# Kernel tuning notes

Hardware: AMD Instinct MI355X
Metric: run time of the kernel (lower is better)

The kernel has to match this reference:

```python
import jax, jax.numpy as jnp
import numpy as np

N_NODES = 20000
N_EDGES = 160000
IN_SIZE = 128
HIDDEN = 256
N_HID_LAYERS = 2
OUT_SIZE = 32
N_GRAPHS = 16
NUM_MP = 4  # BASELINE_MESSAGE_PASSING (weights SHARED across rounds: [Sequential(...)]*N)
NEG_SLOPE = 0.01  # torch.nn.LeakyReLU default
W_SCALE = 0.05


def leaky(x):
    return jnp.where(x >= 0, x, NEG_SLOPE * x)


def wide_mlp(h, Win, bin_, Wh, bh, Wout, bout):
    # Linear(in,H) + act, then N_HID_LAYERS x (Linear(H,H) + act), then Linear(H,out)
    h = leaky(h @ Win + bin_)
    for l in range(Wh.shape[0]):  # small fixed layer count
        h = leaky(h @ Wh[l] + bh[l])
    return h @ Wout + bout


def setup_inputs() -> dict:
    key = jax.random.key(0)
    ks = jax.random.split(key, 16)
    d = {
        "x": jax.random.normal(ks[0], (N_NODES, IN_SIZE), jnp.float32),
        "edge_index": jax.random.randint(ks[1], (2, N_EDGES), 0, N_NODES, jnp.int64),
        "batch": jnp.sort(jax.random.randint(ks[2], (N_NODES,), 0, N_GRAPHS, jnp.int64)),
        "enc_Win": W_SCALE * jax.random.normal(ks[3], (IN_SIZE, HIDDEN), jnp.float32),
        "enc_bin": jnp.zeros((HIDDEN,), jnp.float32),
        "enc_Wh": W_SCALE * jax.random.normal(ks[4], (N_HID_LAYERS, HIDDEN, HIDDEN), jnp.float32),
        "enc_bh": jnp.zeros((N_HID_LAYERS, HIDDEN), jnp.float32),
        "enc_Wout": W_SCALE * jax.random.normal(ks[5], (HIDDEN, HIDDEN), jnp.float32),
        "enc_bout": jnp.zeros((HIDDEN,), jnp.float32),
        "edge_W": W_SCALE * jax.random.normal(ks[6], (3 * HIDDEN, HIDDEN), jnp.float32),
        "edge_b": jnp.zeros((HIDDEN,), jnp.float32),
        "proc_Win": W_SCALE * jax.random.normal(ks[7], (HIDDEN, HIDDEN), jnp.float32),
        "proc_bin": jnp.zeros((HIDDEN,), jnp.float32),
        "proc_Wh": W_SCALE * jax.random.normal(ks[8], (N_HID_LAYERS, HIDDEN, HIDDEN), jnp.float32),
        "proc_bh": jnp.zeros((N_HID_LAYERS, HIDDEN), jnp.float32),
        "proc_Wout": W_SCALE * jax.random.normal(ks[9], (HIDDEN, HIDDEN), jnp.float32),
        "proc_bout": jnp.zeros((HIDDEN,), jnp.float32),
        "dec_Win": W_SCALE * jax.random.normal(ks[10], (3 * HIDDEN, HIDDEN), jnp.float32),
        "dec_bin": jnp.zeros((HIDDEN,), jnp.float32),
        "dec_Wh": W_SCALE * jax.random.normal(ks[11], (N_HID_LAYERS, HIDDEN, HIDDEN), jnp.float32),
        "dec_bh": jnp.zeros((N_HID_LAYERS, HIDDEN), jnp.float32),
        "dec_Wout": W_SCALE * jax.random.normal(ks[12], (HIDDEN, OUT_SIZE), jnp.float32),
        "dec_bout": jnp.zeros((OUT_SIZE,), jnp.float32),
    }
    return d


def reference(x, edge_index, batch,
              enc_Win, enc_bin, enc_Wh, enc_bh, enc_Wout, enc_bout,
              edge_W, edge_b,
              proc_Win, proc_bin, proc_Wh, proc_bh, proc_Wout, proc_bout,
              dec_Win, dec_bin, dec_Wh, dec_bh, dec_Wout, dec_bout):
    n = x.shape[0]
    # encode
    h = wide_mlp(x, enc_Win, enc_bin, enc_Wh, enc_bh, enc_Wout, enc_bout)
    # add_self_loops
    loops = jnp.arange(n, dtype=edge_index.dtype)
    ei = jnp.concatenate([edge_index, jnp.stack([loops, loops])], axis=1)
    src, dst = ei[0], ei[1]  # PyG: j = ei[0] (source), i = ei[1] (target/aggregation index)
    e = jnp.zeros((ei.shape[1], HIDDEN), h.dtype)  # edge_attr None branch -> zeros
    # BASELINE_MESSAGE_PASSING rounds, shared weights
    for _ in range(NUM_MP):
        m = jnp.concatenate([h[dst], h[src], e], axis=-1) @ edge_W + edge_b  # [E+N, H]
        h = jax.ops.segment_sum(m, dst, num_segments=n)  # aggr='add'
        h = wide_mlp(h, proc_Win, proc_bin, proc_Wh, proc_bh, proc_Wout, proc_bout)
    # global mean / max / add pooling over graphs
    sums = jax.ops.segment_sum(h, batch, num_segments=N_GRAPHS)
    cnt = jax.ops.segment_sum(jnp.ones((n, 1), h.dtype), batch, num_segments=N_GRAPHS)
    mean = sums / jnp.maximum(cnt, 1.0)
    mx = jax.ops.segment_max(h, batch, num_segments=N_GRAPHS)
    pooled = jnp.concatenate([mean, mx, sums], axis=-1)  # [G, 3H]
    out = wide_mlp(pooled, dec_Win, dec_bin, dec_Wh, dec_bh, dec_Wout, dec_bout)
    return out
```

## Files before the change

### kernel.cpp

```cpp
#include <hip/hip_runtime.h>
#include <hip/hip_bf16.h>
#include <cstdint>

#define HID 256
#define NGRAPH 16
#define NEG_SLOPE 0.01f

typedef __bf16 bf16x8 __attribute__((ext_vector_type(8)));
typedef float f32x4 __attribute__((ext_vector_type(4)));

__device__ __forceinline__ float leaky(float x) { return x >= 0.f ? x : NEG_SLOPE * x; }

__device__ __forceinline__ ushort f2b(float f) {
  uint u = __float_as_uint(f);
  uint r = (u + 0x7fffu + ((u >> 16) & 1u)) >> 16;
  return (ushort)r;
}
__device__ __forceinline__ float b2f(ushort b) { return __uint_as_float((uint)b << 16); }

__global__ __launch_bounds__(256) void k_zero_i32(int* p, int n) {
  int i = blockIdx.x * blockDim.x + threadIdx.x;
  if (i < n) p[i] = 0;
}

__global__ __launch_bounds__(256) void k_hist(const int* __restrict__ key, int* __restrict__ cnt, int ne) {
  int e = blockIdx.x * blockDim.x + threadIdx.x;
  if (e < ne) atomicAdd(&cnt[key[e]], 1);
}

__global__ __launch_bounds__(1024) void k_scan(const int* __restrict__ cnt, int* __restrict__ rowptr,
                                               int* __restrict__ cursor, int n) {
  __shared__ int sd[1024];
  int tid = threadIdx.x;
  int CH = n / 1024 + 1;
  int base = tid * CH;
  int s = 0;
  for (int i = 0; i < CH; ++i) { int idx = base + i; if (idx < n) s += cnt[idx]; }
  sd[tid] = s;
  __syncthreads();
  for (int off = 1; off < 1024; off <<= 1) {
    int v = (tid >= off) ? sd[tid - off] : 0;
    __syncthreads();
    sd[tid] += v;
    __syncthreads();
  }
  int run = (tid == 0) ? 0 : sd[tid - 1];
  for (int i = 0; i < CH; ++i) {
    int idx = base + i;
    if (idx <= n) {
      rowptr[idx] = run;
      if (idx < n) { cursor[idx] = run; run += cnt[idx]; }
    }
  }
}

__global__ __launch_bounds__(64) void k_gbounds(const int* __restrict__ batch, int n,
                                                int* __restrict__ gstart, int* __restrict__ gcnt) {
  int t = threadIdx.x;
  if (t <= NGRAPH) {
    int lo = 0, hi = n;
    while (lo < hi) { int mid = (lo + hi) >> 1; if (batch[mid] < t) lo = mid + 1; else hi = mid; }
    gstart[t] = lo;
  }
  __syncthreads();
  if (t < NGRAPH) gcnt[t] = gstart[t + 1] - gstart[t];
}

__global__ __launch_bounds__(256) void k_scatter(const int* __restrict__ src, const int* __restrict__ dst,
                                                 int* __restrict__ cursor, int* __restrict__ col, int ne) {
  int e = blockIdx.x * blockDim.x + threadIdx.x;
  if (e < ne) {
    int d = dst[e];
    int pos = atomicAdd(&cursor[d], 1);
    col[pos] = src[e];
  }
}

__global__ __launch_bounds__(256) void k_f2b(const float* __restrict__ src, ushort* __restrict__ dst, int nElem) {
  int i = (blockIdx.x * 256 + threadIdx.x) * 4;
  if (i + 3 < nElem) {
    float4 v = *(const float4*)&src[i];
    ushort4 o;
    o.x = f2b(v.x); o.y = f2b(v.y); o.z = f2b(v.z); o.w = f2b(v.w);
    *(ushort4*)&dst[i] = o;
  } else {
    for (int j = i; j < nElem; ++j) dst[j] = f2b(src[j]);
  }
}

struct WconvArgs {
  const float* src[9];
  ushort* dst[9];
  int K[9];
};

__global__ __launch_bounds__(256) void k_wconv_all(WconvArgs args) {
  __shared__ float t[32][33];
  const int e = blockIdx.z;
  const int K = args.K[e];
  const int k0 = blockIdx.x * 32;
  if (k0 >= K) return;
  const float* src = args.src[e];
  ushort* dst = args.dst[e];
  const int n0 = blockIdx.y * 32;
  const int tx = threadIdx.x & 31;
  const int ty = threadIdx.x >> 5;
#pragma unroll
  for (int r = 0; r < 4; ++r) t[ty + 8 * r][tx] = src[(size_t)(k0 + ty + 8 * r) * 256 + n0 + tx];
  __syncthreads();
#pragma unroll
  for (int r = 0; r < 4; ++r) dst[(size_t)(n0 + ty + 8 * r) * K + k0 + tx] = f2b(t[tx][ty + 8 * r]);
}

__global__ __launch_bounds__(256) void k_aggregate(const ushort* __restrict__ h, const int* __restrict__ rowptr,
                                                   const int* __restrict__ col, ushort* __restrict__ S,
                                                   ushort* __restrict__ hd, float* __restrict__ degf, int n) {
  int node = blockIdx.x * 4 + (threadIdx.x >> 6);
  if (node >= n) return;
  int lane = threadIdx.x & 63;
  const ushort4* h4 = (const ushort4*)h;
  size_t base = (size_t)node * 64 + lane;
  ushort4 self = h4[base];
  float a0 = b2f(self.x), a1 = b2f(self.y), a2 = b2f(self.z), a3 = b2f(self.w);
  float s0 = a0, s1 = a1, s2 = a2, s3 = a3;
  int beg = rowptr[node], end = rowptr[node + 1];
  int p = beg;
  for (; p + 4 <= end; p += 4) {
    int j0 = col[p], j1 = col[p + 1], j2 = col[p + 2], j3 = col[p + 3];
    ushort4 v0 = h4[(size_t)j0 * 64 + lane];
    ushort4 v1 = h4[(size_t)j1 * 64 + lane];
    ushort4 v2 = h4[(size_t)j2 * 64 + lane];
    ushort4 v3 = h4[(size_t)j3 * 64 + lane];
    s0 += b2f(v0.x) + b2f(v1.x) + b2f(v2.x) + b2f(v3.x);
    s1 += b2f(v0.y) + b2f(v1.y) + b2f(v2.y) + b2f(v3.y);
    s2 += b2f(v0.z) + b2f(v1.z) + b2f(v2.z) + b2f(v3.z);
    s3 += b2f(v0.w) + b2f(v1.w) + b2f(v2.w) + b2f(v3.w);
  }
  for (; p < end; ++p) {
    int j = col[p];
    ushort4 v = h4[(size_t)j * 64 + lane];
    s0 += b2f(v.x); s1 += b2f(v.y); s2 += b2f(v.z); s3 += b2f(v.w);
  }
  float deg = (float)(end - beg + 1);
  ushort4 so; so.x = f2b(s0); so.y = f2b(s1); so.z = f2b(s2); so.w = f2b(s3);
  ((ushort4*)S)[base] = so;
  ushort4 ho; ho.x = f2b(deg * a0); ho.y = f2b(deg * a1); ho.z = f2b(deg * a2); ho.w = f2b(deg * a3);
  ((ushort4*)hd)[base] = ho;
  if (lane == 0) degf[node] = deg;
}

struct MLPArgs {
  const ushort* A0;
  const ushort* A1;
  const ushort* W0b;
  const ushort* W[5];
  const float* bias[5];
  const float* degf;
  ushort* out;
  int ldw0;
  int actf[5];
};

template <int NL, int K0, bool DUAL>
__global__ __launch_bounds__(256, 2) void k_mlp(MLPArgs args, int M) {
  __shared__ ushort act[8 * 64 * 32];
  __shared__ __align__(16) ushort As[2][64 * 32];
  __shared__ __align__(16) ushort Bs[2][256 * 32];
  __shared__ float degs[64];

  const int m0 = blockIdx.x * 64;
  const int tid = threadIdx.x;
  const int lane = tid & 63;
  const int wn = tid >> 6;
  const int rl = lane & 15;
  const int kg = lane >> 4;

  if (DUAL && tid < 64) {
    int rr = m0 + tid; if (rr > M - 1) rr = M - 1;
    degs[tid] = args.degf[rr];
  }

  const int s_row = tid >> 2;
  const int s_kg = (tid & 3) ^ ((s_row >> 1) & 3);
  int ga = m0 + s_row; if (ga > M - 1) ga = M - 1;

#define STAGE_A(buf, Ap, k0s)                                                            \
  {                                                                                      \
    const ushort* sa_ = (Ap) + (size_t)ga * K0 + (k0s) + s_kg * 8;                       \
    __builtin_amdgcn_global_load_lds(                                                    \
        (const __attribute__((address_space(1))) void*)sa_,                              \
        (__attribute__((address_space(3))) void*)&As[buf][tid * 8], 16, 0, 0);           \
  }
#define STAGE_B(buf, Wp, ldw, k0s)                                                       \
  _Pragma("unroll")                                                                      \
  for (int i_ = 0; i_ < 4; ++i_) {                                                       \
    const ushort* sb_ = (Wp) + (size_t)(s_row + 64 * i_) * (ldw) + (k0s) + s_kg * 8;     \
    __builtin_amdgcn_global_load_lds(                                                    \
        (const __attribute__((address_space(1))) void*)sb_,                              \
        (__attribute__((address_space(3))) void*)&Bs[buf][(tid + 256 * i_) * 8], 16, 0, 0); \
  }

  int rr_[4], sA_[4], rn_[4], sB_[4];
#pragma unroll
  for (int fm = 0; fm < 4; ++fm) {
    rr_[fm] = fm * 16 + rl;
    sA_[fm] = kg ^ ((rr_[fm] >> 1) & 3);
  }
#pragma unroll
  for (int fn = 0; fn < 4; ++fn) {
    rn_[fn] = wn * 64 + fn * 16 + rl;
    sB_[fn] = kg ^ ((rn_[fn] >> 1) & 3);
  }

  f32x4 acc[4][4];

  auto epilogue = [&](int L, bool toGlobal) {
    const float* bp = args.bias[L];
    const int af_ = args.actf[L];
#pragma unroll
    for (int fn = 0; fn < 4; ++fn) {
      int c = wn * 64 + fn * 16 + rl;
      float bv = bp[c];
      int ch = c >> 5, g = (c >> 3) & 3, e = c & 7;
#pragma unroll
      for (int fm = 0; fm < 4; ++fm) {
        int lrow0 = fm * 16 + kg * 4;
#pragma unroll
        for (int rg = 0; rg < 4; ++rg) {
          int lrow = lrow0 + rg;
          float rs = (DUAL && L == 0) ? degs[lrow] : 1.0f;
          float v = acc[fm][fn][rg] + rs * bv;
          if (af_) v = leaky(v);
          if (toGlobal) {
            int grow = m0 + lrow;
            if (grow < M) args.out[(size_t)grow * 256 + c] = f2b(v);
          } else {
            int slot = g ^ ((lrow >> 1) & 3);
            act[ch * 2048 + lrow * 32 + slot * 8 + e] = f2b(v);
          }
        }
      }
    }
  };

  constexpr int KS0 = K0 >> 5;
  constexpr int NT0 = DUAL ? 2 * KS0 : KS0;
#pragma unroll
  for (int i = 0; i < 4; ++i)
#pragma unroll
    for (int j = 0; j < 4; ++j) acc[i][j] = (f32x4)(0.f);

  STAGE_A(0, args.A0, 0);
  STAGE_B(0, args.W[0], args.ldw0, 0);
  __syncthreads();

#pragma unroll
  for (int t = 0; t < NT0; ++t) {
    if (t + 1 < NT0) {
      const int tp = t + 1;
      const int pass = DUAL ? (tp >= KS0 ? 1 : 0) : 0;
      const int k0s = (tp - pass * KS0) << 5;
      const ushort* Ap = pass ? args.A1 : args.A0;
      const ushort* Wp = pass ? args.W0b : args.W[0];
      STAGE_A(tp & 1, Ap, k0s);
      STAGE_B(tp & 1, Wp, args.ldw0, k0s);
    } else if (NL > 1) {
      STAGE_B(0, args.W[1], 256, 0);
    }
    const ushort* bA = &As[t & 1][0];
    const ushort* bB = &Bs[t & 1][0];
    bf16x8 afr[4], bfr[4];
#pragma unroll
    for (int fm = 0; fm < 4; ++fm) afr[fm] = *(const bf16x8*)&bA[rr_[fm] * 32 + sA_[fm] * 8];
#pragma unroll
    for (int fn = 0; fn < 4; ++fn) bfr[fn] = *(const bf16x8*)&bB[rn_[fn] * 32 + sB_[fn] * 8];
#pragma unroll
    for (int fm = 0; fm < 4; ++fm)
#pragma unroll
      for (int fn = 0; fn < 4; ++fn)
        acc[fm][fn] = __builtin_amdgcn_mfma_f32_16x16x32_bf16(afr[fm], bfr[fn], acc[fm][fn], 0, 0, 0);
    __syncthreads();
  }
  epilogue(0, NL == 1);
  if (NL > 1) __syncthreads();

  for (int L = 1; L < NL; ++L) {
#pragma unroll
    for (int i = 0; i < 4; ++i)
#pragma unroll
      for (int j = 0; j < 4; ++j) acc[i][j] = (f32x4)(0.f);
#pragma unroll
    for (int t = 0; t < 8; ++t) {
      if (t < 7) {
        STAGE_B((t + 1) & 1, args.W[L], 256, (t + 1) * 32);
      } else if (L + 1 < NL) {
        STAGE_B(0, args.W[L + 1], 256, 0);
      }
      const ushort* bB = &Bs[t & 1][0];
      bf16x8 afr[4], bfr[4];
#pragma unroll
      for (int fm = 0; fm < 4; ++fm)
        afr[fm] = *(const bf16x8*)&act[t * 2048 + rr_[fm] * 32 + sA_[fm] * 8];
#pragma unroll
      for (int fn = 0; fn < 4; ++fn) bfr[fn] = *(const bf16x8*)&bB[rn_[fn] * 32 + sB_[fn] * 8];
#pragma unroll
      for (int fm = 0; fm < 4; ++fm)
#pragma unroll
        for (int fn = 0; fn < 4; ++fn)
          acc[fm][fn] = __builtin_amdgcn_mfma_f32_16x16x32_bf16(afr[fm], bfr[fn], acc[fm][fn], 0, 0, 0);
      __syncthreads();
    }
    if (L == NL - 1) {
      epilogue(L, true);
    } else {
      epilogue(L, false);
      __syncthreads();
    }
  }
#undef STAGE_A
#undef STAGE_B
}

__global__ __launch_bounds__(256) void k_dec_layer(
    const float* __restrict__ A, const float* __restrict__ W,
    const float* __restrict__ bias, float* __restrict__ out,
    int K, int N, int act)
{
  __shared__ float a[768];
  __shared__ float red[8][64];
  const int g = blockIdx.y;
  const int cols = (N >= 64) ? 64 : 32;
  const int segs = 256 / cols;
  const int t = threadIdx.x;
  const int col = t % cols, seg = t / cols;
  const int c = blockIdx.x * cols + col;
  for (int i = t; i < K; i += 256) a[i] = A[(size_t)g * K + i];
  __syncthreads();
  const int kper = K / segs;
  const int k0 = seg * kper;
  float p = 0.f;
#pragma unroll 8
  for (int k = k0; k < k0 + kper; ++k) p += a[k] * W[(size_t)k * N + c];
  red[seg][col] = p;
  __syncthreads();
  if (seg == 0) {
    float s = bias[c];
    for (int i = 0; i < segs; ++i) s += red[i][col];
    out[(size_t)g * N + c] = act ? leaky(s) : s;
  }
}

__global__ __launch_bounds__(256) void k_pool1(const ushort* __restrict__ h, const int* __restrict__ gstart,
                                               const int* __restrict__ gcnt, float* __restrict__ psum,
                                               float* __restrict__ pmax) {
  int g = blockIdx.x >> 4;
  int cch = blockIdx.x & 15;
  int t = threadIdx.x;
  int len = gcnt[g];
  int s0 = gstart[g];
  int chunk = (len + 15) >> 4;
  int i0 = s0 + cch * chunk;
  int i1 = min(i0 + chunk, s0 + len);
  float s = 0.f;
  float m = -3.402823466e+38f;
  for (int i = i0; i < i1; ++i) {
    float v = b2f(h[(size_t)i * HID + t]);
    s += v;
    m = fmaxf(m, v);
  }
  psum[(size_t)blockIdx.x * HID + t] = s;
  pmax[(size_t)blockIdx.x * HID + t] = m;
}

__global__ __launch_bounds__(256) void k_pool2(const float* __restrict__ psum, const float* __restrict__ pmax,
                                               const int* __restrict__ gcnt, float* __restrict__ pooled) {
  int g = blockIdx.x;
  int t = threadIdx.x;
  float s = 0.f, m = -3.402823466e+38f;
  for (int cch = 0; cch < 16; ++cch) {
    s += psum[(size_t)(g * 16 + cch) * HID + t];
    m = fmaxf(m, pmax[(size_t)(g * 16 + cch) * HID + t]);
  }
  float cf = (float)gcnt[g];
  pooled[g * 3 * HID + t] = s / fmaxf(cf, 1.f);
  pooled[g * 3 * HID + HID + t] = m;
  pooled[g * 3 * HID + 2 * HID + t] = s;
}

extern "C" void kernel_launch(void* const* d_in, const int* in_sizes, int n_in,
                              void* d_out, int out_size, void* d_ws, size_t ws_size,
                              hipStream_t stream) {
  const float* x        = (const float*)d_in[0];
  const int*   ei       = (const int*)d_in[1];
  const int*   batch    = (const int*)d_in[2];
  const float* enc_Win  = (const float*)d_in[3];
  const float* enc_bin  = (const float*)d_in[4];
  const float* enc_Wh   = (const float*)d_in[5];
  const float* enc_bh   = (const float*)d_in[6];
  const float* enc_Wout = (const float*)d_in[7];
  const float* enc_bout = (const float*)d_in[8];
  const float* edge_W   = (const float*)d_in[9];
  const float* edge_b   = (const float*)d_in[10];
  const float* proc_Win = (const float*)d_in[11];
  const float* proc_bin = (const float*)d_in[12];
  const float* proc_Wh  = (const float*)d_in[13];
  const float* proc_bh  = (const float*)d_in[14];
  const float* proc_Wout= (const float*)d_in[15];
  const float* proc_bout= (const float*)d_in[16];
  const float* dec_Win  = (const float*)d_in[17];
  const float* dec_bin  = (const float*)d_in[18];
  const float* dec_Wh   = (const float*)d_in[19];
  const float* dec_bh   = (const float*)d_in[20];
  const float* dec_Wout = (const float*)d_in[21];
  const float* dec_bout = (const float*)d_in[22];

  const int n  = in_sizes[0] / 128;
  const int ne = in_sizes[1] / 2;
  const int H = HID;

  char* p = (char*)d_ws;
  auto alloc = [&](size_t bytes) -> char* {
    char* r = p;
    p += (bytes + 255) & ~(size_t)255;
    return r;
  };
  ushort* hb1   = (ushort*)alloc((size_t)n * H * 2);
  ushort* Sb    = (ushort*)alloc((size_t)n * H * 2);
  ushort* hdb   = (ushort*)alloc((size_t)n * H * 2);
  ushort* xb    = (ushort*)alloc((size_t)n * 128 * 2);
  ushort* w_enc_in  = (ushort*)alloc((size_t)256 * 128 * 2);
  ushort* w_enc_h0  = (ushort*)alloc((size_t)256 * 256 * 2);
  ushort* w_enc_h1  = (ushort*)alloc((size_t)256 * 256 * 2);
  ushort* w_enc_out = (ushort*)alloc((size_t)256 * 256 * 2);
  ushort* w_proc_in  = (ushort*)alloc((size_t)256 * 256 * 2);
  ushort* w_proc_h0  = (ushort*)alloc((size_t)256 * 256 * 2);
  ushort* w_proc_h1  = (ushort*)alloc((size_t)256 * 256 * 2);
  ushort* w_proc_out = (ushort*)alloc((size_t)256 * 256 * 2);
  ushort* w_edge     = (ushort*)alloc((size_t)256 * 512 * 2);
  float* degf   = (float*)alloc((size_t)n * 4);
  float* pooled = (float*)alloc((size_t)NGRAPH * 3 * H * 4);
  float* psum   = (float*)alloc((size_t)256 * H * 4);
  float* pmax   = (float*)alloc((size_t)256 * H * 4);
  float* db0    = (float*)alloc((size_t)NGRAPH * H * 4);
  float* db1    = (float*)alloc((size_t)NGRAPH * H * 4);
  int* cnt    = (int*)alloc((size_t)n * 4);
  int* rowptr = (int*)alloc((size_t)(n + 1) * 4);
  int* cursor = (int*)alloc((size_t)n * 4);
  int* gstart = (int*)alloc((size_t)(NGRAPH + 1) * 4);
  int* gcnt   = (int*)alloc((size_t)NGRAPH * 4);
  int* colv   = (int*)alloc((size_t)ne * 4);

  const int* srcI = ei;
  const int* dstI = ei + ne;

  dim3 blk(256);

  WconvArgs wa;
  wa.src[0] = enc_Win;             wa.dst[0] = w_enc_in;   wa.K[0] = 128;
  wa.src[1] = enc_Wh;              wa.dst[1] = w_enc_h0;   wa.K[1] = 256;
  wa.src[2] = enc_Wh + 65536;      wa.dst[2] = w_enc_h1;   wa.K[2] = 256;
  wa.src[3] = enc_Wout;            wa.dst[3] = w_enc_out;  wa.K[3] = 256;
  wa.src[4] = proc_Win;            wa.dst[4] = w_proc_in;  wa.K[4] = 256;
  wa.src[5] = proc_Wh;             wa.dst[5] = w_proc_h0;  wa.K[5] = 256;
  wa.src[6] = proc_Wh + 65536;     wa.dst[6] = w_proc_h1;  wa.K[6] = 256;
  wa.src[7] = proc_Wout;           wa.dst[7] = w_proc_out; wa.K[7] = 256;
  wa.src[8] = edge_W;              wa.dst[8] = w_edge;     wa.K[8] = 512;
  k_wconv_all<<<dim3(16, 8, 9), blk, 0, stream>>>(wa);
  k_f2b<<<dim3((n * 128 / 4 + 255) / 256), blk, 0, stream>>>(x, xb, n * 128);

  k_zero_i32<<<dim3((n + 255) / 256), blk, 0, stream>>>(cnt, n);
  k_hist<<<dim3((ne + 255) / 256), blk, 0, stream>>>(dstI, cnt, ne);
  k_scan<<<1, 1024, 0, stream>>>(cnt, rowptr, cursor, n);
  k_gbounds<<<1, 64, 0, stream>>>(batch, n, gstart, gcnt);
  k_scatter<<<dim3((ne + 255) / 256), blk, 0, stream>>>(srcI, dstI, cursor, colv, ne);

  const int npanel = (n + 63) / 64;

  MLPArgs ea = {};
  ea.A0 = xb; ea.A1 = nullptr; ea.W0b = nullptr;
  ea.W[0] = w_enc_in; ea.W[1] = w_enc_h0; ea.W[2] = w_enc_h1; ea.W[3] = w_enc_out;
  ea.bias[0] = enc_bin; ea.bias[1] = enc_bh; ea.bias[2] = enc_bh + 256; ea.bias[3] = enc_bout;
  ea.degf = nullptr; ea.out = hb1; ea.ldw0 = 128;
  ea.actf[0] = 1; ea.actf[1] = 1; ea.actf[2] = 1; ea.actf[3] = 0;
  k_mlp<4, 128, false><<<dim3(npanel), blk, 0, stream>>>(ea, n);

  MLPArgs pa = {};
  pa.A0 = hdb; pa.A1 = Sb; pa.W0b = w_edge + 256;
  pa.W[0] = w_edge; pa.W[1] = w_proc_in; pa.W[2] = w_proc_h0; pa.W[3] = w_proc_h1; pa.W[4] = w_proc_out;
  pa.bias[0] = edge_b; pa.bias[1] = proc_bin; pa.bias[2] = proc_bh; pa.bias[3] = proc_bh + 256; pa.bias[4] = proc_bout;
  pa.degf = degf; pa.out = hb1; pa.ldw0 = 512;
  pa.actf[0] = 0; pa.actf[1] = 1; pa.actf[2] = 1; pa.actf[3] = 1; pa.actf[4] = 0;

  for (int r = 0; r < 4; ++r) {
    k_aggregate<<<dim3((n + 3) / 4), blk, 0, stream>>>(hb1, rowptr, colv, Sb, hdb, degf, n);
    k_mlp<5, 256, true><<<dim3(npanel), blk, 0, stream>>>(pa, n);
  }

  k_pool1<<<dim3(NGRAPH * 16), blk, 0, stream>>>(hb1, gstart, gcnt, psum, pmax);
  k_pool2<<<dim3(NGRAPH), blk, 0, stream>>>(psum, pmax, gcnt, pooled);

  k_dec_layer<<<dim3(4, NGRAPH), blk, 0, stream>>>(pooled, dec_Win, dec_bin, db0, 768, 256, 1);
  k_dec_layer<<<dim3(4, NGRAPH), blk, 0, stream>>>(db0, dec_Wh, dec_bh, db1, 256, 256, 1);
  k_dec_layer<<<dim3(4, NGRAPH), blk, 0, stream>>>(db1, dec_Wh + 65536, dec_bh + 256, db0, 256, 256, 1);
  k_dec_layer<<<dim3(1, NGRAPH), blk, 0, stream>>>(db0, dec_Wout, dec_bout, (float*)d_out, 256, 32, 0);
}
```

Baseline: 416.3 us.

## Deepen MLP kernel load pipeline with multi-buffered LDS and unified stage loop

Replaces the double-buffered per-layer GEMM loops in the fused MLP kernel with one flattened stage loop across all layers. A is triple-buffered and B quad-buffered, with loads issued two stages ahead and partial vmcnt waits plus raw s_barrier in place of full __syncthreads. This lets weight prefetch run across layer boundaries and hide global-to-LDS latency. LDS use grows (about 100KB) and the occupancy hint of 2 blocks per SM is dropped, so fewer blocks may be resident, and the hand-written waitcnt counts must be exactly right for correctness.

New measurement: 832.3 us. 99.9% more time.

```diff
diff --git a/kernel.cpp b/kernel.cpp
--- a/kernel.cpp
+++ b/kernel.cpp
@@ -162,10 +162,14 @@
 };
 
 template <int NL, int K0, bool DUAL>
-__global__ __launch_bounds__(256, 2) void k_mlp(MLPArgs args, int M) {
+__global__ __launch_bounds__(256) void k_mlp(MLPArgs args, int M) {
+  constexpr int KS0 = K0 >> 5;
+  constexpr int NT0 = (DUAL ? 2 : 1) * KS0;
+  constexpr int TOTAL = NT0 + 8 * (NL - 1);
+
   __shared__ ushort act[8 * 64 * 32];
-  __shared__ __align__(16) ushort As[2][64 * 32];
-  __shared__ __align__(16) ushort Bs[2][256 * 32];
+  __shared__ __align__(16) ushort As[3][64 * 32];
+  __shared__ __align__(16) ushort Bs[4][256 * 32];
   __shared__ float degs[64];
 
   const int m0 = blockIdx.x * 64;
@@ -181,24 +185,46 @@
   }
 
   const int s_row = tid >> 2;
-  const int s_kg = (tid & 3) ^ ((s_row >> 1) & 3);
+  const int s_sl = tid & 3;
+  const int s_kg = s_sl ^ ((s_row >> 1) & 3);
   int ga = m0 + s_row; if (ga > M - 1) ga = M - 1;
 
-#define STAGE_A(buf, Ap, k0s)                                                            \
-  {                                                                                      \
-    const ushort* sa_ = (Ap) + (size_t)ga * K0 + (k0s) + s_kg * 8;                       \
-    __builtin_amdgcn_global_load_lds(                                                    \
-        (const __attribute__((address_space(1))) void*)sa_,                              \
-        (__attribute__((address_space(3))) void*)&As[buf][tid * 8], 16, 0, 0);           \
-  }
-#define STAGE_B(buf, Wp, ldw, k0s)                                                       \
-  _Pragma("unroll")                                                                      \
-  for (int i_ = 0; i_ < 4; ++i_) {                                                       \
-    const ushort* sb_ = (Wp) + (size_t)(s_row + 64 * i_) * (ldw) + (k0s) + s_kg * 8;     \
-    __builtin_amdgcn_global_load_lds(                                                    \
-        (const __attribute__((address_space(1))) void*)sb_,                              \
-        (__attribute__((address_space(3))) void*)&Bs[buf][(tid + 256 * i_) * 8], 16, 0, 0); \
-  }
+  auto stageA = [&](int s) {
+    int ss = (s < NT0) ? s : 0;
+    int pass = (DUAL && ss >= KS0) ? 1 : 0;
+    int ko = (ss - pass * KS0) << 5;
+    const ushort* Ap = pass ? args.A1 : args.A0;
+    const ushort* src = Ap + (size_t)ga * K0 + ko + s_kg * 8;
+    __builtin_amdgcn_global_load_lds(
+        (const __attribute__((address_space(1))) void*)src,
+        (__attribute__((address_space(3))) void*)&As[s % 3][tid * 8], 16, 0, 0);
+  };
+  auto stageB = [&](int s) {
+    const ushort* Wp; int ldw, ko;
+    if (s < NT0) {
+      int pass = (DUAL && s >= KS0) ? 1 : 0;
+      Wp = pass ? args.W0b : args.W[0];
+      ldw = args.ldw0;
+      ko = (s - pass * KS0) << 5;
+    } else {
+      int q = s - NT0;
+      int L = 1 + (q >> 3);
+      if (L >= NL) { L = NL - 1; ko = 0; }
+      else ko = (q & 7) << 5;
+      Wp = args.W[L];
+      ldw = 256;
+    }
+    ushort* dst = &Bs[s & 3][0];
+#pragma unroll
+    for (int i = 0; i < 4; ++i) {
+      int row = s_row + 64 * i;
+      int kgi = s_sl ^ ((row >> 1) & 3);
+      const ushort* src = Wp + (size_t)row * ldw + ko + kgi * 8;
+      __builtin_amdgcn_global_load_lds(
+          (const __attribute__((address_space(1))) void*)src,
+          (__attribute__((address_space(3))) void*)&dst[(tid + 256 * i) * 8], 16, 0, 0);
+    }
+  };
 
   int rr_[4], sA_[4], rn_[4], sB_[4];
 #pragma unroll
@@ -213,6 +239,10 @@
   }
 
   f32x4 acc[4][4];
+#pragma unroll
+  for (int i = 0; i < 4; ++i)
+#pragma unroll
+    for (int j = 0; j < 4; ++j) acc[i][j] = (f32x4)(0.f);
 
   auto epilogue = [&](int L, bool toGlobal) {
     const float* bp = args.bias[L];
@@ -243,35 +273,28 @@
     }
   };
 
-  constexpr int KS0 = K0 >> 5;
-  constexpr int NT0 = DUAL ? 2 * KS0 : KS0;
-#pragma unroll
-  for (int i = 0; i < 4; ++i)
-#pragma unroll
-    for (int j = 0; j < 4; ++j) acc[i][j] = (f32x4)(0.f);
-
-  STAGE_A(0, args.A0, 0);
-  STAGE_B(0, args.W[0], args.ldw0, 0);
-  __syncthreads();
-
-#pragma unroll
-  for (int t = 0; t < NT0; ++t) {
-    if (t + 1 < NT0) {
-      const int tp = t + 1;
-      const int pass = DUAL ? (tp >= KS0 ? 1 : 0) : 0;
-      const int k0s = (tp - pass * KS0) << 5;
-      const ushort* Ap = pass ? args.A1 : args.A0;
-      const ushort* Wp = pass ? args.W0b : args.W[0];
-      STAGE_A(tp & 1, Ap, k0s);
-      STAGE_B(tp & 1, Wp, args.ldw0, k0s);
-    } else if (NL > 1) {
-      STAGE_B(0, args.W[1], 256, 0);
+  stageA(0);
+  stageB(0);
+  stageB(1);
+  asm volatile("s_waitcnt lgkmcnt(0)" ::: "memory");
+
+  for (int s = 0; s < TOTAL; ++s) {
+    stageA(s + 1);
+    stageB(s + 2);
+    asm volatile("s_waitcnt vmcnt(9)\n\ts_barrier" ::: "memory");
+
+    const ushort* bB = &Bs[s & 3][0];
+    bf16x8 afr[4], bfr[4];
+    if (s < NT0) {
+      const ushort* bA = &As[s % 3][0];
+#pragma unroll
+      for (int fm = 0; fm < 4; ++fm) afr[fm] = *(const bf16x8*)&bA[rr_[fm] * 32 + sA_[fm] * 8];
+    } else {
+      int t = (s - NT0) & 7;
+#pragma unroll
+      for (int fm = 0; fm < 4; ++fm)
+        afr[fm] = *(const bf16x8*)&act[t * 2048 + rr_[fm] * 32 + sA_[fm] * 8];
     }
-    const ushort* bA = &As[t & 1][0];
-    const ushort* bB = &Bs[t & 1][0];
-    bf16x8 afr[4], bfr[4];
-#pragma unroll
-    for (int fm = 0; fm < 4; ++fm) afr[fm] = *(const bf16x8*)&bA[rr_[fm] * 32 + sA_[fm] * 8];
 #pragma unroll
     for (int fn = 0; fn < 4; ++fn) bfr[fn] = *(const bf16x8*)&bB[rn_[fn] * 32 + sB_[fn] * 8];
 #pragma unroll
@@ -279,46 +302,23 @@
 #pragma unroll
       for (int fn = 0; fn < 4; ++fn)
         acc[fm][fn] = __builtin_amdgcn_mfma_f32_16x16x32_bf16(afr[fm], bfr[fn], acc[fm][fn], 0, 0, 0);
-    __syncthreads();
-  }
-  epilogue(0, NL == 1);
-  if (NL > 1) __syncthreads();
-
-  for (int L = 1; L < NL; ++L) {
-#pragma unroll
-    for (int i = 0; i < 4; ++i)
-#pragma unroll
-      for (int j = 0; j < 4; ++j) acc[i][j] = (f32x4)(0.f);
-#pragma unroll
-    for (int t = 0; t < 8; ++t) {
-      if (t < 7) {
-        STAGE_B((t + 1) & 1, args.W[L], 256, (t + 1) * 32);
-      } else if (L + 1 < NL) {
-        STAGE_B(0, args.W[L + 1], 256, 0);
+
+    bool lend = (s < NT0) ? (s == NT0 - 1) : (((s - NT0) & 7) == 7);
+    if (lend) {
+      int Lcur = (s < NT0) ? 0 : 1 + ((s - NT0) >> 3);
+      asm volatile("s_barrier" ::: "memory");
+      if (Lcur == NL - 1) {
+        epilogue(Lcur, true);
+      } else {
+        epilogue(Lcur, false);
+        asm volatile("s_waitcnt lgkmcnt(0)\n\ts_barrier" ::: "memory");
+#pragma unroll
+        for (int i = 0; i < 4; ++i)
+#pragma unroll
+          for (int j = 0; j < 4; ++j) acc[i][j] = (f32x4)(0.f);
       }
-      const ushort* bB = &Bs[t & 1][0];
-      bf16x8 afr[4], bfr[4];
-#pragma unroll
-      for (int fm = 0; fm < 4; ++fm)
-        afr[fm] = *(const bf16x8*)&act[t * 2048 + rr_[fm] * 32 + sA_[fm] * 8];
-#pragma unroll
-      for (int fn = 0; fn < 4; ++fn) bfr[fn] = *(const bf16x8*)&bB[rn_[fn] * 32 + sB_[fn] * 8];
-#pragma unroll
-      for (int fm = 0; fm < 4; ++fm)
-#pragma unroll
-        for (int fn = 0; fn < 4; ++fn)
-          acc[fm][fn] = __builtin_amdgcn_mfma_f32_16x16x32_bf16(afr[fm], bfr[fn], acc[fm][fn], 0, 0, 0);
-      __syncthreads();
     }
-    if (L == NL - 1) {
-      epilogue(L, true);
-    } else {
-      epilogue(L, false);
-      __syncthreads();
-    }
-  }
-#undef STAGE_A
-#undef STAGE_B
+  }
 }
 
 __global__ __launch_bounds__(256) void k_dec_layer(
```
